# Kernel optimization log

Measured on AMD Instinct MI355X. Metric: run time of the kernel, lower is better.

## Reference

```python
import jax, jax.numpy as jnp
import numpy as np

B, T_ENC, T_DEC = 32, 128, 32
V_SRC, V_TGT = 32000, 32000
E_SRC, E_TGT = 256, 256
H_ENC, H_DEC, A = 512, 512, 8
CTX = 2 * H_ENC  # bidirectional encoder output dim


def setup_inputs():
    key = jax.random.key(0)
    ks = jax.random.split(key, 24)
    s = jnp.float32(0.02)

    def rn(k, shape):
        return jax.random.normal(k, shape, jnp.float32) * s

    return {
        'encoder_inputs': jax.random.randint(ks[0], (B, T_ENC), 0, V_SRC),
        'encoder_seq_length': jax.random.randint(ks[1], (B,), 1, T_ENC + 1),
        'decoder_inputs': jax.random.randint(ks[2], (B, T_DEC), 0, V_TGT),
        'decoder_seq_length': jax.random.randint(ks[3], (B,), 1, T_DEC + 1),
        'emb_src': rn(ks[4], (V_SRC, E_SRC)).at[0].set(0.0),  # padding_idx=0
        'emb_tgt': rn(ks[5], (V_TGT, E_TGT)).at[0].set(0.0),
        'Wih_f': rn(ks[6], (4 * H_ENC, E_SRC)), 'Whh_f': rn(ks[7], (4 * H_ENC, H_ENC)),
        'bih_f': rn(ks[8], (4 * H_ENC,)), 'bhh_f': rn(ks[9], (4 * H_ENC,)),
        'Wih_b': rn(ks[10], (4 * H_ENC, E_SRC)), 'Whh_b': rn(ks[11], (4 * H_ENC, H_ENC)),
        'bih_b': rn(ks[12], (4 * H_ENC,)), 'bhh_b': rn(ks[13], (4 * H_ENC,)),
        'gru_Wih': rn(ks[14], (3 * H_DEC, E_TGT + CTX)), 'gru_Whh': rn(ks[15], (3 * H_DEC, H_DEC)),
        'gru_bih': rn(ks[16], (3 * H_DEC,)), 'gru_bhh': rn(ks[17], (3 * H_DEC,)),
        'attn_W': rn(ks[18], (CTX + H_DEC, A)), 'attn_b': rn(ks[19], (A,)),
        'attn_v': rn(ks[20], (A,)),
        'clf_W': rn(ks[21], (V_TGT, H_DEC)), 'clf_b': rn(ks[22], (V_TGT,)),
    }


def _lstm(x_tbe, Wih, Whh, bih, bhh):
    # x_tbe: [T, B, E] -> hidden outputs [T, B, H]; PyTorch gate order i,f,g,o
    Bz = x_tbe.shape[1]
    h0 = jnp.zeros((Bz, H_ENC), x_tbe.dtype)

    def step(carry, xt):
        h, c = carry
        g = xt @ Wih.T + bih + h @ Whh.T + bhh
        i, f, gg, o = jnp.split(g, 4, axis=-1)
        c = jax.nn.sigmoid(f) * c + jax.nn.sigmoid(i) * jnp.tanh(gg)
        h = jax.nn.sigmoid(o) * jnp.tanh(c)
        return (h, c), h

    _, hs = jax.lax.scan(step, (h0, h0), x_tbe)
    return hs


def _gru(x, h, Wih, Whh, bih, bhh):
    # PyTorch GRUCell: gates r, z, n
    gi = x @ Wih.T + bih
    gh = h @ Whh.T + bhh
    ir, iz, inn = jnp.split(gi, 3, axis=-1)
    hr, hz, hn = jnp.split(gh, 3, axis=-1)
    r = jax.nn.sigmoid(ir + hr)
    z = jax.nn.sigmoid(iz + hz)
    n = jnp.tanh(inn + r * hn)
    return (1.0 - z) * n + z * h


def reference(encoder_inputs, encoder_seq_length, decoder_inputs, decoder_seq_length,
              emb_src, emb_tgt,
              Wih_f, Whh_f, bih_f, bhh_f, Wih_b, Whh_b, bih_b, bhh_b,
              gru_Wih, gru_Whh, gru_bih, gru_bhh,
              attn_W, attn_b, attn_v, clf_W, clf_b):
    lens = encoder_seq_length
    x = emb_src[encoder_inputs]                                   # [B,T,E]
    t = jnp.arange(T_ENC)[None, :]
    valid = t < lens[:, None]                                     # [B,T]

    # forward LSTM (padded steps masked out below; they never affect valid outputs)
    h_f = jnp.swapaxes(_lstm(jnp.swapaxes(x, 0, 1), Wih_f, Whh_f, bih_f, bhh_f), 0, 1)
    # backward LSTM: reverse each sequence within its true length
    rev = jnp.where(valid, lens[:, None] - 1 - t, t)              # [B,T]
    x_r = jnp.take_along_axis(x, rev[:, :, None], axis=1)
    h_b = jnp.swapaxes(_lstm(jnp.swapaxes(x_r, 0, 1), Wih_b, Whh_b, bih_b, bhh_b), 0, 1)
    h_b = jnp.take_along_axis(h_b, rev[:, :, None], axis=1)
    # pad_packed_sequence zeroes outputs past seq length
    enc_out = jnp.concatenate([h_f, h_b], axis=-1) * valid[:, :, None].astype(x.dtype)  # [B,T,2H]

    NEG = jnp.float32(-1e9)

    def step(h, tok):
        # ConcatAttention: v^T tanh(W [enc_out; state] + b), masked softmax
        feat = jnp.concatenate(
            [enc_out, jnp.broadcast_to(h[:, None, :], (B, T_ENC, H_DEC))], axis=-1)
        e = jnp.tanh(feat @ attn_W + attn_b) @ attn_v             # [B,T]
        a = jax.nn.softmax(jnp.where(valid, e, NEG), axis=-1)
        ctx = jnp.einsum('bt,btd->bd', a, enc_out)                # [B,2H]
        # pre-concat decoder: GRUCell([emb; ctx], h)
        xin = jnp.concatenate([emb_tgt[tok], ctx], axis=-1)
        h_new = _gru(xin, h, gru_Wih, gru_Whh, gru_bih, gru_bhh)
        logit = jax.nn.relu(h_new @ clf_W.T + clf_b)              # [B,V]
        return h_new, logit

    h0 = jnp.zeros((B, H_DEC), jnp.float32)
    _, outs = jax.lax.scan(step, h0, jnp.swapaxes(decoder_inputs, 0, 1))
    return jnp.swapaxes(outs, 0, 1)                               # [B,T_dec,V_tgt]
```

## Files before the change

kernel.cpp:

```cpp
#include <hip/hip_runtime.h>
#include <cmath>

#define NB   32
#define TE   128
#define TD   32
#define VOC  32000
#define EMB  256
#define HH   512
#define CTXD 1024
#define NR   1536

#define OHS  8192
#define OEO  (OHS + 2*129*NB*HH)
#define OEP  (OEO + NB*TE*CTXD)
#define OHD  (OEP + NB*TE*8)
#define OVEO (OHD + (TD+1)*NB*HH)
#define WSEND (OVEO + NB*NR*TE/2)

typedef __attribute__((ext_vector_type(8))) short bf16x8;
typedef __attribute__((ext_vector_type(4))) float f32x4;

__device__ __forceinline__ float sigf(float x) { return 1.0f / (1.0f + expf(-x)); }
__device__ __forceinline__ float hsum4(float4 v) { return (v.x + v.y) + (v.z + v.w); }

__device__ __forceinline__ void stg1(float* p, float v) {
  __hip_atomic_store(p, v, __ATOMIC_RELAXED, __HIP_MEMORY_SCOPE_AGENT);
}

__device__ __forceinline__ void fma4(float4& a, const float4 w, const float4 u) {
  a.x = fmaf(w.x, u.x, a.x); a.y = fmaf(w.y, u.y, a.y);
  a.z = fmaf(w.z, u.z, a.z); a.w = fmaf(w.w, u.w, a.w);
}

__device__ __forceinline__ unsigned short to_bf16(float f) {
  unsigned int u = __float_as_uint(f);
  u = (u + 0x7FFF + ((u >> 16) & 1)) >> 16;
  return (unsigned short)u;
}

__device__ __forceinline__ void gbarG(int* bar, int idx, int target) {
  __syncthreads();
  if (threadIdx.x == 0) {
    __hip_atomic_fetch_add(bar + (idx & 7) * 16, 1,
                           __ATOMIC_RELAXED, __HIP_MEMORY_SCOPE_AGENT);
  }
  if (threadIdx.x < 64) {
    const int ln = threadIdx.x;
    int it = 0;
    while (true) {
      int v = (ln < 8)
        ? __hip_atomic_load(bar + ln * 16, __ATOMIC_RELAXED, __HIP_MEMORY_SCOPE_AGENT)
        : 0;
      v += __shfl_xor(v, 1); v += __shfl_xor(v, 2); v += __shfl_xor(v, 4);
      v = __shfl(v, 0);
      if (v >= target) break;
      __builtin_amdgcn_s_sleep(1);
      if (++it > (1 << 20)) break;
    }
  }
  __syncthreads();
}

__global__ void __launch_bounds__(512)
scan_kernel(const int* __restrict__ enc_in, const int* __restrict__ lens,
            const float* __restrict__ emb_src,
            const float* __restrict__ Wih_f, const float* __restrict__ Whh_f,
            const float* __restrict__ bih_f, const float* __restrict__ bhh_f,
            const float* __restrict__ Wih_b, const float* __restrict__ Whh_b,
            const float* __restrict__ bih_b, const float* __restrict__ bhh_b,
            float* __restrict__ ws)
{
  const int tid = threadIdx.x, bid = blockIdx.x;
  const int g = bid & 7, cg = bid >> 3;
  const int dir = g >> 2, bg = g & 3;
  int* flg = (int*)ws + g * 512;
  float* harr = ws + OHS;
  float* eo   = ws + OEO;

  asm volatile("buffer_inv sc1" ::: "memory");

  __shared__ int   tokL[TE][8];
  __shared__ float lds_p[8][4][68];

  for (int i = tid; i < TE * 8; i += 512) {
    int bb = i & 7, s = i >> 3;
    int b = bg * 8 + bb;
    int t = s;
    if (dir) { int L = lens[b]; t = (s < L) ? (L - 1 - s) : s; }
    tokL[s][bb] = enc_in[b * TE + t];
  }
  if (tid < 128) {
    int bb = tid >> 4, col = tid & 15;
    stg1(&harr[((size_t)(dir * 129) * NB + bg * 8 + bb) * HH + cg * 16 + col], 0.0f);
  }

  const int lane = tid & 63, w = tid >> 6;
  const int ks = w & 3, rh = w >> 2;
  const int rq = lane >> 4, kl = lane & 15;
  const int j0 = cg * 16;
  const float* Wih = dir ? Wih_b : Wih_f;
  const float* Whh = dir ? Whh_b : Whh_f;

  float4 Wreg[8][3];
  #pragma unroll
  for (int ri = 0; ri < 8; ++ri) {
    int r = rh * 32 + rq * 8 + ri;
    int o = (r >> 4) * HH + j0 + (r & 15);
    #pragma unroll
    for (int p = 0; p < 3; ++p) {
      int kf = (ks * 3 + p) * 16 + kl;
      Wreg[ri][p] = (kf < 64)
        ? *((const float4*)Wih + (size_t)o * 64 + kf)
        : *((const float4*)Whh + (size_t)o * 128 + (kf - 64));
    }
  }

  const int b_u = tid >> 4, col_u = tid & 15;
  const int j_u = j0 + col_u;
  const int bglob = bg * 8 + b_u;
  const int Lu = (tid < 128) ? lens[bglob] : 0;
  float bs0 = 0, bs1 = 0, bs2 = 0, bs3 = 0;
  if (tid < 128) {
    const float* bih = dir ? bih_b : bih_f;
    const float* bhh = dir ? bhh_b : bhh_f;
    bs0 = bih[j_u] + bhh[j_u];
    bs1 = bih[HH + j_u] + bhh[HH + j_u];
    bs2 = bih[2 * HH + j_u] + bhh[2 * HH + j_u];
    bs3 = bih[3 * HH + j_u] + bhh[3 * HH + j_u];
  }
  float cst = 0.0f;

  const int pbase = (ks == 1) ? 0 : (ks == 2) ? 8 : 20;
  const int pnum  = (ks == 1) ? 8 : 12;

  __syncthreads();
  if (tid == 0)
    __hip_atomic_store(flg + cg * 16, 1, __ATOMIC_RELAXED, __HIP_MEMORY_SCOPE_AGENT);

  for (int s = 0; s < TE; ++s) {
    if (ks != 0) {
      int it = 0;
      while (true) {
        int v = (lane < pnum)
          ? __hip_atomic_load(flg + (pbase + lane) * 16,
                              __ATOMIC_RELAXED, __HIP_MEMORY_SCOPE_AGENT)
          : 0x7fffffff;
        v = min(v, __shfl_xor(v, 1));  v = min(v, __shfl_xor(v, 2));
        v = min(v, __shfl_xor(v, 4));  v = min(v, __shfl_xor(v, 8));
        v = min(v, __shfl_xor(v, 16)); v = min(v, __shfl_xor(v, 32));
        if (v >= s + 1) break;
        __builtin_amdgcn_s_sleep(1);
        if (++it > (1 << 20)) break;
      }
    }

    const float4* h4 = (const float4*)(harr + ((size_t)(dir * 129 + s) * NB) * HH);
    #pragma unroll 2
    for (int bb = 0; bb < 8; ++bb) {
      const int b = bg * 8 + bb;
      const int tok = tokL[s][bb];
      const float4* x4 = (const float4*)emb_src + (size_t)tok * 64;
      float4 u[3];
      #pragma unroll
      for (int p = 0; p < 3; ++p) {
        int c = ks * 3 + p;
        u[p] = (c < 4) ? x4[c * 16 + kl]
                       : h4[(size_t)b * 128 + (c - 4) * 16 + kl];
      }
      float sc[8];
      #pragma unroll
      for (int ri = 0; ri < 8; ++ri) {
        float4 a = {0, 0, 0, 0};
        fma4(a, Wreg[ri][0], u[0]);
        fma4(a, Wreg[ri][1], u[1]);
        fma4(a, Wreg[ri][2], u[2]);
        sc[ri] = hsum4(a);
      }
      #pragma unroll
      for (int ri = 0; ri < 8; ++ri) {
        sc[ri] += __shfl_xor(sc[ri], 1);
        sc[ri] += __shfl_xor(sc[ri], 2);
        sc[ri] += __shfl_xor(sc[ri], 4);
        sc[ri] += __shfl_xor(sc[ri], 8);
      }
      if (kl == 0) {
        int r0 = rh * 32 + rq * 8;
        float4 lo = {sc[0], sc[1], sc[2], sc[3]};
        float4 hi = {sc[4], sc[5], sc[6], sc[7]};
        *(float4*)&lds_p[bb][ks][r0]     = lo;
        *(float4*)&lds_p[bb][ks][r0 + 4] = hi;
      }
    }
    __syncthreads();

    if (tid < 128) {
      float gi = bs0, gf = bs1, gg = bs2, go = bs3;
      #pragma unroll
      for (int k2 = 0; k2 < 4; ++k2) {
        gi += lds_p[b_u][k2][col_u];
        gf += lds_p[b_u][k2][16 + col_u];
        gg += lds_p[b_u][k2][32 + col_u];
        go += lds_p[b_u][k2][48 + col_u];
      }
      float c = sigf(gf) * cst + sigf(gi) * tanhf(gg);
      cst = c;
      float h = sigf(go) * tanhf(c);
      stg1(&harr[((size_t)(dir * 129 + s + 1) * NB + bglob) * HH + j_u], h);
      float hm = (s < Lu) ? h : 0.0f;
      int pos = dir ? ((s < Lu) ? (Lu - 1 - s) : s) : s;
      eo[((size_t)bglob * TE + pos) * CTXD + dir * HH + j_u] = hm;
    }
    __syncthreads();
    if (tid == 0)
      __hip_atomic_store(flg + cg * 16, s + 2,
                         __ATOMIC_RELAXED, __HIP_MEMORY_SCOPE_AGENT);
  }
}

__global__ void __launch_bounds__(256)
veo_kernel(const float* __restrict__ eo, const float* __restrict__ gWih,
           unsigned short* __restrict__ veo)
{
  asm volatile("buffer_inv sc1" ::: "memory");
  __shared__ __align__(16) float As[16][132];
  __shared__ __align__(16) float Bs[16][132];
  const int tid = threadIdx.x;
  const int tx = tid & 15, ty = tid >> 4;
  const int n0 = blockIdx.x * 128, m0 = blockIdx.y * 128;
  float acc[8][8] = {};
  const int lr = tid >> 1;
  const int lk = (tid & 1) * 8;
  const float* arow = eo + (size_t)(m0 + lr) * CTXD;
  const float* brow = gWih + (size_t)(n0 + lr) * (EMB + CTXD) + EMB;

  for (int kc = 0; kc < CTXD; kc += 16) {
    float4 av0 = *(const float4*)&arow[kc + lk];
    float4 av1 = *(const float4*)&arow[kc + lk + 4];
    float4 bv0 = *(const float4*)&brow[kc + lk];
    float4 bv1 = *(const float4*)&brow[kc + lk + 4];
    __syncthreads();
    As[lk + 0][lr] = av0.x; As[lk + 1][lr] = av0.y;
    As[lk + 2][lr] = av0.z; As[lk + 3][lr] = av0.w;
    As[lk + 4][lr] = av1.x; As[lk + 5][lr] = av1.y;
    As[lk + 6][lr] = av1.z; As[lk + 7][lr] = av1.w;
    Bs[lk + 0][lr] = bv0.x; Bs[lk + 1][lr] = bv0.y;
    Bs[lk + 2][lr] = bv0.z; Bs[lk + 3][lr] = bv0.w;
    Bs[lk + 4][lr] = bv1.x; Bs[lk + 5][lr] = bv1.y;
    Bs[lk + 6][lr] = bv1.z; Bs[lk + 7][lr] = bv1.w;
    __syncthreads();
    #pragma unroll
    for (int kk = 0; kk < 16; ++kk) {
      float a8[8], b8[8];
      *(float4*)&a8[0] = *(const float4*)&As[kk][ty * 8];
      *(float4*)&a8[4] = *(const float4*)&As[kk][ty * 8 + 4];
      *(float4*)&b8[0] = *(const float4*)&Bs[kk][tx * 8];
      *(float4*)&b8[4] = *(const float4*)&Bs[kk][tx * 8 + 4];
      #pragma unroll
      for (int i = 0; i < 8; ++i)
        #pragma unroll
        for (int j = 0; j < 8; ++j)
          acc[i][j] = fmaf(a8[i], b8[j], acc[i][j]);
    }
  }
  const int b = m0 >> 7;
  #pragma unroll
  for (int j = 0; j < 8; ++j) {
    int n = n0 + tx * 8 + j;
    unsigned short o8[8];
    #pragma unroll
    for (int i = 0; i < 8; ++i) o8[i] = to_bf16(acc[i][j]);
    *(uint4*)&veo[((size_t)b * NR + n) * TE + ty * 8] = *(uint4*)o8;
  }
}

__global__ void __launch_bounds__(512)
dec_kernel(const int* __restrict__ dec_in, const int* __restrict__ lens,
           const float* __restrict__ emb_tgt,
           const float* __restrict__ gWih, const float* __restrict__ gWhh,
           const float* __restrict__ gbih, const float* __restrict__ gbhh,
           const float* __restrict__ attn_W, const float* __restrict__ attn_b,
           const float* __restrict__ attn_v,
           float* __restrict__ ws)
{
  const int tid = threadIdx.x, bid = blockIdx.x;
  const int g = bid & 7, cg = bid >> 3;
  const int B4 = g * 4;
  int* bar = (int*)ws + 4096 + g * 128;
  float* eo = ws + OEO;
  float* ep = ws + OEP;
  float* hd = ws + OHD;
  const unsigned short* veoH = (const unsigned short*)(ws + OVEO);

  asm volatile("buffer_inv sc1" ::: "memory");

  __shared__ float hl[4][520];
  __shared__ int   tokD[TD][4];
  __shared__ int   lensh[4];
  __shared__ float av8v[8];
  __shared__ float hpv[4][8];
  __shared__ float elds[4][128];
  __shared__ float wlds[4][128];
  __shared__ float mxs[4], invs[4];
  __shared__ float gvc[4][48];
  __shared__ float lds_pd[2][4][4][52];

  for (int i = tid; i < TD * 4; i += 512)
    tokD[i >> 2][i & 3] = dec_in[(B4 + (i & 3)) * TD + (i >> 2)];
  if (tid < 8) av8v[tid] = attn_v[tid];
  if (tid < 4) lensh[tid] = lens[B4 + tid];

  if (tid < 64) {
    int bb = tid >> 4, col = tid & 15;
    stg1(&hd[(size_t)(B4 + bb) * HH + cg * 16 + col], 0.0f);
  }

  {
    const int idx = cg * 512 + tid;
    if (idx < 4 * TE * 8) {
      int a = idx & 7, t = (idx >> 3) & 127, bb = idx >> 10;
      int b = B4 + bb;
      float acc = attn_b[a];
      const float* er = &eo[((size_t)b * TE + t) * CTXD];
      for (int d = 0; d < CTXD; d += 4) {
        float4 ev = *(const float4*)&er[d];
        acc = fmaf(ev.x, attn_W[(d + 0) * 8 + a], acc);
        acc = fmaf(ev.y, attn_W[(d + 1) * 8 + a], acc);
        acc = fmaf(ev.z, attn_W[(d + 2) * 8 + a], acc);
        acc = fmaf(ev.w, attn_W[(d + 3) * 8 + a], acc);
      }
      stg1(&ep[((size_t)b * TE + t) * 8 + a], acc);
    }
  }

  const int lane = tid & 63, w = tid >> 6;
  const int ks = w & 3, rh = w >> 2;
  const int rq = lane >> 4, kl = lane & 15;
  float4 Wreg[6][3];
  #pragma unroll
  for (int ri = 0; ri < 6; ++ri) {
    int rr = rh * 24 + rq * 6 + ri;
    int row = (rr >> 4) * HH + cg * 16 + (rr & 15);
    #pragma unroll
    for (int p = 0; p < 3; ++p) {
      int c = ks * 3 + p;
      Wreg[ri][p] = (c < 4)
        ? *(const float4*)(gWih + (size_t)row * (EMB + CTXD) + c * 64 + kl * 4)
        : *(const float4*)(gWhh + (size_t)row * HH + (c - 4) * 64 + kl * 4);
    }
  }

  const int ub = tid >> 4, ucol = tid & 15;
  const int uj = cg * 16 + ucol;
  float bRc = 0, bZc = 0, bNi = 0, bNh = 0;
  if (tid < 64) {
    bRc = gbih[uj] + gbhh[uj];
    bZc = gbih[HH + uj] + gbhh[HH + uj];
    bNi = gbih[2 * HH + uj];
    bNh = gbhh[2 * HH + uj];
  }

  int tgt = 32;
  gbarG(bar, cg, tgt); tgt += 32;

  for (int s = 0; s < TD; ++s) {
    {
      int bb = tid >> 7, c4 = (tid & 127) * 4;
      *(float4*)&hl[bb][c4] =
        *(const float4*)&hd[((size_t)s * NB + B4 + bb) * HH + c4];
    }
    __syncthreads();
    {
      const int bb = w >> 1;
      const float4* h4 = (const float4*)&hl[bb][0];
      float4 ha = h4[lane * 2], hb = h4[lane * 2 + 1];
      #pragma unroll
      for (int i = 0; i < 4; ++i) {
        const int a = (w & 1) * 4 + i;
        const float* wa = attn_W + (size_t)(CTXD + lane * 8) * 8 + a;
        float acc = 0.0f;
        acc = fmaf(ha.x, wa[0],  acc); acc = fmaf(ha.y, wa[8],  acc);
        acc = fmaf(ha.z, wa[16], acc); acc = fmaf(ha.w, wa[24], acc);
        acc = fmaf(hb.x, wa[32], acc); acc = fmaf(hb.y, wa[40], acc);
        acc = fmaf(hb.z, wa[48], acc); acc = fmaf(hb.w, wa[56], acc);
        acc += __shfl_xor(acc, 1);  acc += __shfl_xor(acc, 2);
        acc += __shfl_xor(acc, 4);  acc += __shfl_xor(acc, 8);
        acc += __shfl_xor(acc, 16); acc += __shfl_xor(acc, 32);
        if (lane == 0) hpv[bb][a] = acc;
      }
    }
    __syncthreads();
    {
      const int bb = tid >> 7, t = tid & 127;
      const int b = B4 + bb;
      float evv = -1e9f;
      if (t < lensh[bb]) {
        const float* e8 = &ep[((size_t)b * TE + t) * 8];
        float4 ea = *(const float4*)e8, eb2 = *(const float4*)(e8 + 4);
        evv  = tanhf(ea.x + hpv[bb][0]) * av8v[0];
        evv += tanhf(ea.y + hpv[bb][1]) * av8v[1];
        evv += tanhf(ea.z + hpv[bb][2]) * av8v[2];
        evv += tanhf(ea.w + hpv[bb][3]) * av8v[3];
        evv += tanhf(eb2.x + hpv[bb][4]) * av8v[4];
        evv += tanhf(eb2.y + hpv[bb][5]) * av8v[5];
        evv += tanhf(eb2.z + hpv[bb][6]) * av8v[6];
        evv += tanhf(eb2.w + hpv[bb][7]) * av8v[7];
      }
      elds[bb][t] = evv;
    }
    __syncthreads();
    if (tid < 256) {
      const int bb = tid >> 6, i = tid & 63;
      float m = fmaxf(elds[bb][i], elds[bb][i + 64]);
      m = fmaxf(m, __shfl_xor(m, 1));  m = fmaxf(m, __shfl_xor(m, 2));
      m = fmaxf(m, __shfl_xor(m, 4));  m = fmaxf(m, __shfl_xor(m, 8));
      m = fmaxf(m, __shfl_xor(m, 16)); m = fmaxf(m, __shfl_xor(m, 32));
      if (i == 0) mxs[bb] = m;
    }
    __syncthreads();
    {
      const int bb = tid >> 7, t = tid & 127;
      wlds[bb][t] = expf(elds[bb][t] - mxs[bb]);
    }
    __syncthreads();
    if (tid < 256) {
      const int bb = tid >> 6, i = tid & 63;
      float sm = wlds[bb][i] + wlds[bb][i + 64];
      sm += __shfl_xor(sm, 1);  sm += __shfl_xor(sm, 2);
      sm += __shfl_xor(sm, 4);  sm += __shfl_xor(sm, 8);
      sm += __shfl_xor(sm, 16); sm += __shfl_xor(sm, 32);
      if (i == 0) invs[bb] = 1.0f / sm;
    }
    {
      #pragma unroll
      for (int bb = 0; bb < 4; ++bb) {
        const float4* xr = (const float4*)(emb_tgt + (size_t)tokD[s][bb] * EMB);
        float4 u[3];
        #pragma unroll
        for (int p = 0; p < 3; ++p) {
          int c = ks * 3 + p;
          u[p] = (c < 4) ? xr[c * 16 + kl]
                         : *(const float4*)&hl[bb][(c - 4) * 64 + kl * 4];
        }
        float sI[6], sH[6];
        #pragma unroll
        for (int ri = 0; ri < 6; ++ri) {
          float4 aI = {0,0,0,0}, aH = {0,0,0,0};
          #pragma unroll
          for (int p = 0; p < 3; ++p) {
            int c = ks * 3 + p;
            if (c < 4) fma4(aI, Wreg[ri][p], u[p]);
            else       fma4(aH, Wreg[ri][p], u[p]);
          }
          sI[ri] = hsum4(aI); sH[ri] = hsum4(aH);
        }
        #pragma unroll
        for (int ri = 0; ri < 6; ++ri) {
          sI[ri] += __shfl_xor(sI[ri], 1); sH[ri] += __shfl_xor(sH[ri], 1);
          sI[ri] += __shfl_xor(sI[ri], 2); sH[ri] += __shfl_xor(sH[ri], 2);
          sI[ri] += __shfl_xor(sI[ri], 4); sH[ri] += __shfl_xor(sH[ri], 4);
          sI[ri] += __shfl_xor(sI[ri], 8); sH[ri] += __shfl_xor(sH[ri], 8);
        }
        if (kl == 0) {
          int r0 = rh * 24 + rq * 6;
          #pragma unroll
          for (int ri = 0; ri < 6; ++ri) {
            lds_pd[0][bb][ks][r0 + ri] = sI[ri];
            lds_pd[1][bb][ks][r0 + ri] = sH[ri];
          }
        }
      }
    }
    __syncthreads();
    if (tid < 384) {
      const int bb = tid / 96, idx = tid % 96;
      const int rr = idx >> 1, th = idx & 1;
      const int n = (rr >> 4) * HH + cg * 16 + (rr & 15);
      const unsigned short* vp = veoH + ((size_t)(B4 + bb) * NR + n) * TE + th * 64;
      const float* wl = &wlds[bb][th * 64];
      float acc = 0.0f;
      #pragma unroll
      for (int q = 0; q < 8; ++q) {
        uint4 pk = *(const uint4*)&vp[q * 8];
        unsigned int uu[4] = {pk.x, pk.y, pk.z, pk.w};
        #pragma unroll
        for (int h2 = 0; h2 < 4; ++h2) {
          acc = fmaf(wl[q * 8 + h2 * 2 + 0],
                     __uint_as_float((uu[h2] & 0xFFFFu) << 16), acc);
          acc = fmaf(wl[q * 8 + h2 * 2 + 1],
                     __uint_as_float((uu[h2] >> 16) << 16), acc);
        }
      }
      acc += __shfl_xor(acc, 1);
      if (th == 0) gvc[bb][rr] = acc * invs[bb];
    }
    __syncthreads();
    if (tid < 64) {
      float giR = gvc[ub][ucol], ghR = 0;
      float giZ = gvc[ub][16 + ucol], ghZ = 0;
      float giN = gvc[ub][32 + ucol], ghN = 0;
      #pragma unroll
      for (int k2 = 0; k2 < 4; ++k2) {
        giR += lds_pd[0][ub][k2][ucol];      ghR += lds_pd[1][ub][k2][ucol];
        giZ += lds_pd[0][ub][k2][16 + ucol]; ghZ += lds_pd[1][ub][k2][16 + ucol];
        giN += lds_pd[0][ub][k2][32 + ucol]; ghN += lds_pd[1][ub][k2][32 + ucol];
      }
      float r = sigf(giR + ghR + bRc);
      float z = sigf(giZ + ghZ + bZc);
      float n = tanhf(giN + bNi + r * (ghN + bNh));
      float hnew = (1.0f - z) * n + z * hl[ub][uj];
      stg1(&hd[((size_t)(s + 1) * NB + B4 + ub) * HH + uj], hnew);
    }
    gbarG(bar, cg, tgt); tgt += 32;
  }
}

__global__ void __launch_bounds__(256)
conv_kernel(const float* __restrict__ hd,
            unsigned short* __restrict__ Abh, unsigned short* __restrict__ Abl)
{
  asm volatile("buffer_inv sc1" ::: "memory");
  const int idx = blockIdx.x * 256 + threadIdx.x;
  const int m = idx >> 6;
  const int k8 = (idx & 63) * 8;
  const float* src = hd + ((size_t)((m & 31) + 1) * NB + (m >> 5)) * HH + k8;
  float4 a0 = *(const float4*)src;
  float4 a1 = *(const float4*)(src + 4);
  float f[8] = {a0.x, a0.y, a0.z, a0.w, a1.x, a1.y, a1.z, a1.w};
  unsigned short hi[8], lo[8];
  #pragma unroll
  for (int i = 0; i < 8; ++i) {
    unsigned short h = to_bf16(f[i]);
    float fh = __uint_as_float(((unsigned int)h) << 16);
    hi[i] = h;
    lo[i] = to_bf16(f[i] - fh);
  }
  *(uint4*)&Abh[(size_t)m * HH + k8] = *(uint4*)hi;
  *(uint4*)&Abl[(size_t)m * HH + k8] = *(uint4*)lo;
}

__global__ void __launch_bounds__(256)
clf_kernel(const unsigned short* __restrict__ Abh, const unsigned short* __restrict__ Abl,
           const float* __restrict__ W, const float* __restrict__ bias,
           float* __restrict__ out)
{
  asm volatile("buffer_inv sc1" ::: "memory");
  __shared__ __align__(16) unsigned short Ah[256][40];
  __shared__ __align__(16) unsigned short Al[256][40];
  __shared__ __align__(16) unsigned short Wh[128][40];
  const int tid = threadIdx.x;
  const int wv = tid >> 6, l = tid & 63;
  const int lr = l & 15, lkq = l >> 4;
  const int n0 = blockIdx.x * 128, m0 = blockIdx.y * 256;
  f32x4 acc[2][16] = {};

  for (int kc = 0; kc < HH; kc += 32) {
    __syncthreads();
    {
      const unsigned short* sh = Abh + (size_t)(m0 + tid) * HH + kc;
      const unsigned short* sl = Abl + (size_t)(m0 + tid) * HH + kc;
      uint4 h0 = *(const uint4*)(sh);      uint4 h1 = *(const uint4*)(sh + 8);
      uint4 h2 = *(const uint4*)(sh + 16); uint4 h3 = *(const uint4*)(sh + 24);
      uint4 l0 = *(const uint4*)(sl);      uint4 l1 = *(const uint4*)(sl + 8);
      uint4 l2 = *(const uint4*)(sl + 16); uint4 l3 = *(const uint4*)(sl + 24);
      *(uint4*)&Ah[tid][0]  = h0; *(uint4*)&Ah[tid][8]  = h1;
      *(uint4*)&Ah[tid][16] = h2; *(uint4*)&Ah[tid][24] = h3;
      *(uint4*)&Al[tid][0]  = l0; *(uint4*)&Al[tid][8]  = l1;
      *(uint4*)&Al[tid][16] = l2; *(uint4*)&Al[tid][24] = l3;
      const int wr = tid >> 1, hf = tid & 1;
      const float* wsrc = W + (size_t)(n0 + wr) * HH + kc + hf * 16;
      unsigned int o[8];
      #pragma unroll
      for (int i = 0; i < 16; i += 4) {
        float4 v = *(const float4*)&wsrc[i];
        o[(i >> 1) + 0] = (unsigned int)to_bf16(v.x) | ((unsigned int)to_bf16(v.y) << 16);
        o[(i >> 1) + 1] = (unsigned int)to_bf16(v.z) | ((unsigned int)to_bf16(v.w) << 16);
      }
      *(uint4*)&Wh[wr][hf * 16]     = *(uint4*)&o[0];
      *(uint4*)&Wh[wr][hf * 16 + 8] = *(uint4*)&o[4];
    }
    __syncthreads();
    bf16x8 bfr[2];
    bfr[0] = *(const bf16x8*)&Wh[wv * 32 + lr][lkq * 8];
    bfr[1] = *(const bf16x8*)&Wh[wv * 32 + 16 + lr][lkq * 8];
    #pragma unroll
    for (int mf = 0; mf < 16; ++mf) {
      bf16x8 ah = *(const bf16x8*)&Ah[mf * 16 + lr][lkq * 8];
      bf16x8 al = *(const bf16x8*)&Al[mf * 16 + lr][lkq * 8];
      #pragma unroll
      for (int nf = 0; nf < 2; ++nf) {
        acc[nf][mf] = __builtin_amdgcn_mfma_f32_16x16x32_bf16(ah, bfr[nf], acc[nf][mf], 0, 0, 0);
        acc[nf][mf] = __builtin_amdgcn_mfma_f32_16x16x32_bf16(al, bfr[nf], acc[nf][mf], 0, 0, 0);
      }
    }
  }
  #pragma unroll
  for (int nf = 0; nf < 2; ++nf) {
    const int n = n0 + wv * 32 + nf * 16 + lr;
    const float bn = bias[n];
    #pragma unroll
    for (int mf = 0; mf < 16; ++mf) {
      #pragma unroll
      for (int r = 0; r < 4; ++r) {
        int m = m0 + mf * 16 + lkq * 4 + r;
        out[(size_t)m * VOC + n] = fmaxf(acc[nf][mf][r] + bn, 0.0f);
      }
    }
  }
}

extern "C" void kernel_launch(void* const* d_in, const int* in_sizes, int n_in,
                              void* d_out, int out_size, void* d_ws, size_t ws_size,
                              hipStream_t stream)
{
  if (ws_size < (size_t)WSEND * 4) return;

  const int* enc_in  = (const int*)d_in[0];
  const int* enc_len = (const int*)d_in[1];
  const int* dec_in  = (const int*)d_in[2];
  const float* emb_src = (const float*)d_in[4];
  const float* emb_tgt = (const float*)d_in[5];
  const float* Wih_f = (const float*)d_in[6];
  const float* Whh_f = (const float*)d_in[7];
  const float* bih_f = (const float*)d_in[8];
  const float* bhh_f = (const float*)d_in[9];
  const float* Wih_b = (const float*)d_in[10];
  const float* Whh_b = (const float*)d_in[11];
  const float* bih_b = (const float*)d_in[12];
  const float* bhh_b = (const float*)d_in[13];
  const float* gWih  = (const float*)d_in[14];
  const float* gWhh  = (const float*)d_in[15];
  const float* gbih  = (const float*)d_in[16];
  const float* gbhh  = (const float*)d_in[17];
  const float* attn_W = (const float*)d_in[18];
  const float* attn_b = (const float*)d_in[19];
  const float* attn_v = (const float*)d_in[20];
  const float* clf_W = (const float*)d_in[21];
  const float* clf_b = (const float*)d_in[22];
  float* ws  = (float*)d_ws;
  float* out = (float*)d_out;

  unsigned short* Abh = (unsigned short*)(ws + OHS);
  unsigned short* Abl = Abh + (size_t)NB * TD * HH;

  hipMemsetAsync(d_ws, 0, 20480, stream);
  scan_kernel<<<256, 512, 0, stream>>>(enc_in, enc_len, emb_src,
      Wih_f, Whh_f, bih_f, bhh_f, Wih_b, Whh_b, bih_b, bhh_b, ws);
  veo_kernel<<<dim3(NR / 128, (NB * TE) / 128), 256, 0, stream>>>(
      ws + OEO, gWih, (unsigned short*)(ws + OVEO));
  dec_kernel<<<256, 512, 0, stream>>>(dec_in, enc_len, emb_tgt,
      gWih, gWhh, gbih, gbhh, attn_W, attn_b, attn_v, ws);
  conv_kernel<<<256, 256, 0, stream>>>(ws + OHD, Abh, Abl);
  dim3 cg(VOC / 128, (NB * TD) / 256);
  clf_kernel<<<cg, 256, 0, stream>>>(Abh, Abl, clf_W, clf_b, out);
}
```

Before: 2.009 ms.

## Warp-specialize decoder step to overlap attention softmax with GRU dot products

The decoder step is split across warp groups. Warps 0-3 each compute one batch row's attention projection, scores, max and softmax entirely in registers with wave shuffles, while warps 4-7 run their share of the GRU input and hidden dot products. The two groups then swap: warps 0-3 run their GRU dots and warps 4-7 compute the bf16 context projection. This removes several block-wide barriers and LDS round trips per step (the hpv, elds and mxs buffers) and overlaps independent work. The cost is that the context reduction now runs on fewer threads with a longer serial loop, and the two phases may be unevenly balanced.

```diff
diff --git a/kernel.cpp b/kernel.cpp
--- a/kernel.cpp
+++ b/kernel.cpp
@@ -297,10 +297,8 @@
   __shared__ int   tokD[TD][4];
   __shared__ int   lensh[4];
   __shared__ float av8v[8];
-  __shared__ float hpv[4][8];
-  __shared__ float elds[4][128];
   __shared__ float wlds[4][128];
-  __shared__ float mxs[4], invs[4];
+  __shared__ float invs[4];
   __shared__ float gvc[4][48];
   __shared__ float lds_pd[2][4][4][52];
 
@@ -359,6 +357,47 @@
     bNh = gbhh[2 * HH + uj];
   }
 
+  auto DOTS = [&](int s) {
+    #pragma unroll
+    for (int bb = 0; bb < 4; ++bb) {
+      const float4* xr = (const float4*)(emb_tgt + (size_t)tokD[s][bb] * EMB);
+      float4 u[3];
+      #pragma unroll
+      for (int p = 0; p < 3; ++p) {
+        int c = ks * 3 + p;
+        u[p] = (c < 4) ? xr[c * 16 + kl]
+                       : *(const float4*)&hl[bb][(c - 4) * 64 + kl * 4];
+      }
+      float sI[6], sH[6];
+      #pragma unroll
+      for (int ri = 0; ri < 6; ++ri) {
+        float4 aI = {0,0,0,0}, aH = {0,0,0,0};
+        #pragma unroll
+        for (int p = 0; p < 3; ++p) {
+          int c = ks * 3 + p;
+          if (c < 4) fma4(aI, Wreg[ri][p], u[p]);
+          else       fma4(aH, Wreg[ri][p], u[p]);
+        }
+        sI[ri] = hsum4(aI); sH[ri] = hsum4(aH);
+      }
+      #pragma unroll
+      for (int ri = 0; ri < 6; ++ri) {
+        sI[ri] += __shfl_xor(sI[ri], 1); sH[ri] += __shfl_xor(sH[ri], 1);
+        sI[ri] += __shfl_xor(sI[ri], 2); sH[ri] += __shfl_xor(sH[ri], 2);
+        sI[ri] += __shfl_xor(sI[ri], 4); sH[ri] += __shfl_xor(sH[ri], 4);
+        sI[ri] += __shfl_xor(sI[ri], 8); sH[ri] += __shfl_xor(sH[ri], 8);
+      }
+      if (kl == 0) {
+        int r0 = rh * 24 + rq * 6;
+        #pragma unroll
+        for (int ri = 0; ri < 6; ++ri) {
+          lds_pd[0][bb][ks][r0 + ri] = sI[ri];
+          lds_pd[1][bb][ks][r0 + ri] = sH[ri];
+        }
+      }
+    }
+  };
+
   int tgt = 32;
   gbarG(bar, cg, tgt); tgt += 32;
 
@@ -369,13 +408,14 @@
         *(const float4*)&hd[((size_t)s * NB + B4 + bb) * HH + c4];
     }
     __syncthreads();
-    {
-      const int bb = w >> 1;
+
+    if (w < 4) {
+      const int bb = w, b = B4 + bb;
       const float4* h4 = (const float4*)&hl[bb][0];
       float4 ha = h4[lane * 2], hb = h4[lane * 2 + 1];
-      #pragma unroll
-      for (int i = 0; i < 4; ++i) {
-        const int a = (w & 1) * 4 + i;
+      float hp[8];
+      #pragma unroll
+      for (int a = 0; a < 8; ++a) {
         const float* wa = attn_W + (size_t)(CTXD + lane * 8) * 8 + a;
         float acc = 0.0f;
         acc = fmaf(ha.x, wa[0],  acc); acc = fmaf(ha.y, wa[8],  acc);
@@ -385,115 +425,77 @@
         acc += __shfl_xor(acc, 1);  acc += __shfl_xor(acc, 2);
         acc += __shfl_xor(acc, 4);  acc += __shfl_xor(acc, 8);
         acc += __shfl_xor(acc, 16); acc += __shfl_xor(acc, 32);
-        if (lane == 0) hpv[bb][a] = acc;
-      }
-    }
-    __syncthreads();
-    {
-      const int bb = tid >> 7, t = tid & 127;
-      const int b = B4 + bb;
-      float evv = -1e9f;
-      if (t < lensh[bb]) {
-        const float* e8 = &ep[((size_t)b * TE + t) * 8];
+        hp[a] = acc;
+      }
+      const int Lb = lensh[bb];
+      float ev0 = -1e9f, ev1 = -1e9f;
+      if (lane < Lb) {
+        const float* e8 = &ep[((size_t)b * TE + lane) * 8];
         float4 ea = *(const float4*)e8, eb2 = *(const float4*)(e8 + 4);
-        evv  = tanhf(ea.x + hpv[bb][0]) * av8v[0];
-        evv += tanhf(ea.y + hpv[bb][1]) * av8v[1];
-        evv += tanhf(ea.z + hpv[bb][2]) * av8v[2];
-        evv += tanhf(ea.w + hpv[bb][3]) * av8v[3];
-        evv += tanhf(eb2.x + hpv[bb][4]) * av8v[4];
-        evv += tanhf(eb2.y + hpv[bb][5]) * av8v[5];
-        evv += tanhf(eb2.z + hpv[bb][6]) * av8v[6];
-        evv += tanhf(eb2.w + hpv[bb][7]) * av8v[7];
-      }
-      elds[bb][t] = evv;
-    }
-    __syncthreads();
-    if (tid < 256) {
-      const int bb = tid >> 6, i = tid & 63;
-      float m = fmaxf(elds[bb][i], elds[bb][i + 64]);
-      m = fmaxf(m, __shfl_xor(m, 1));  m = fmaxf(m, __shfl_xor(m, 2));
-      m = fmaxf(m, __shfl_xor(m, 4));  m = fmaxf(m, __shfl_xor(m, 8));
-      m = fmaxf(m, __shfl_xor(m, 16)); m = fmaxf(m, __shfl_xor(m, 32));
-      if (i == 0) mxs[bb] = m;
-    }
-    __syncthreads();
-    {
-      const int bb = tid >> 7, t = tid & 127;
-      wlds[bb][t] = expf(elds[bb][t] - mxs[bb]);
-    }
-    __syncthreads();
-    if (tid < 256) {
-      const int bb = tid >> 6, i = tid & 63;
-      float sm = wlds[bb][i] + wlds[bb][i + 64];
+        ev0  = tanhf(ea.x + hp[0]) * av8v[0];
+        ev0 += tanhf(ea.y + hp[1]) * av8v[1];
+        ev0 += tanhf(ea.z + hp[2]) * av8v[2];
+        ev0 += tanhf(ea.w + hp[3]) * av8v[3];
+        ev0 += tanhf(eb2.x + hp[4]) * av8v[4];
+        ev0 += tanhf(eb2.y + hp[5]) * av8v[5];
+        ev0 += tanhf(eb2.z + hp[6]) * av8v[6];
+        ev0 += tanhf(eb2.w + hp[7]) * av8v[7];
+      }
+      if (lane + 64 < Lb) {
+        const float* e8 = &ep[((size_t)b * TE + lane + 64) * 8];
+        float4 ea = *(const float4*)e8, eb2 = *(const float4*)(e8 + 4);
+        ev1  = tanhf(ea.x + hp[0]) * av8v[0];
+        ev1 += tanhf(ea.y + hp[1]) * av8v[1];
+        ev1 += tanhf(ea.z + hp[2]) * av8v[2];
+        ev1 += tanhf(ea.w + hp[3]) * av8v[3];
+        ev1 += tanhf(eb2.x + hp[4]) * av8v[4];
+        ev1 += tanhf(eb2.y + hp[5]) * av8v[5];
+        ev1 += tanhf(eb2.z + hp[6]) * av8v[6];
+        ev1 += tanhf(eb2.w + hp[7]) * av8v[7];
+      }
+      float mx = fmaxf(ev0, ev1);
+      mx = fmaxf(mx, __shfl_xor(mx, 1));  mx = fmaxf(mx, __shfl_xor(mx, 2));
+      mx = fmaxf(mx, __shfl_xor(mx, 4));  mx = fmaxf(mx, __shfl_xor(mx, 8));
+      mx = fmaxf(mx, __shfl_xor(mx, 16)); mx = fmaxf(mx, __shfl_xor(mx, 32));
+      float w0 = expf(ev0 - mx), w1 = expf(ev1 - mx);
+      wlds[bb][lane] = w0;
+      wlds[bb][lane + 64] = w1;
+      float sm = w0 + w1;
       sm += __shfl_xor(sm, 1);  sm += __shfl_xor(sm, 2);
       sm += __shfl_xor(sm, 4);  sm += __shfl_xor(sm, 8);
       sm += __shfl_xor(sm, 16); sm += __shfl_xor(sm, 32);
-      if (i == 0) invs[bb] = 1.0f / sm;
-    }
-    {
-      #pragma unroll
-      for (int bb = 0; bb < 4; ++bb) {
-        const float4* xr = (const float4*)(emb_tgt + (size_t)tokD[s][bb] * EMB);
-        float4 u[3];
+      if (lane == 0) invs[bb] = 1.0f / sm;
+    } else {
+      DOTS(s);
+    }
+    __syncthreads();
+
+    if (w < 4) {
+      DOTS(s);
+    } else {
+      const int bb = w - 4;
+      if (lane < 48) {
+        const int rr = lane;
+        const int n = (rr >> 4) * HH + cg * 16 + (rr & 15);
+        const unsigned short* vp = veoH + ((size_t)(B4 + bb) * NR + n) * TE;
+        float acc = 0.0f;
         #pragma unroll
-        for (int p = 0; p < 3; ++p) {
-          int c = ks * 3 + p;
-          u[p] = (c < 4) ? xr[c * 16 + kl]
-                         : *(const float4*)&hl[bb][(c - 4) * 64 + kl * 4];
-        }
-        float sI[6], sH[6];
-        #pragma unroll
-        for (int ri = 0; ri < 6; ++ri) {
-          float4 aI = {0,0,0,0}, aH = {0,0,0,0};
+        for (int q = 0; q < 16; ++q) {
+          uint4 pk = *(const uint4*)&vp[q * 8];
+          unsigned int uu[4] = {pk.x, pk.y, pk.z, pk.w};
           #pragma unroll
-          for (int p = 0; p < 3; ++p) {
-            int c = ks * 3 + p;
-            if (c < 4) fma4(aI, Wreg[ri][p], u[p]);
-            else       fma4(aH, Wreg[ri][p], u[p]);
-          }
-          sI[ri] = hsum4(aI); sH[ri] = hsum4(aH);
-        }
-        #pragma unroll
-        for (int ri = 0; ri < 6; ++ri) {
-          sI[ri] += __shfl_xor(sI[ri], 1); sH[ri] += __shfl_xor(sH[ri], 1);
-          sI[ri] += __shfl_xor(sI[ri], 2); sH[ri] += __shfl_xor(sH[ri], 2);
-          sI[ri] += __shfl_xor(sI[ri], 4); sH[ri] += __shfl_xor(sH[ri], 4);
-          sI[ri] += __shfl_xor(sI[ri], 8); sH[ri] += __shfl_xor(sH[ri], 8);
-        }
-        if (kl == 0) {
-          int r0 = rh * 24 + rq * 6;
-          #pragma unroll
-          for (int ri = 0; ri < 6; ++ri) {
-            lds_pd[0][bb][ks][r0 + ri] = sI[ri];
-            lds_pd[1][bb][ks][r0 + ri] = sH[ri];
+          for (int h2 = 0; h2 < 4; ++h2) {
+            acc = fmaf(wlds[bb][q * 8 + h2 * 2 + 0],
+                       __uint_as_float((uu[h2] & 0xFFFFu) << 16), acc);
+            acc = fmaf(wlds[bb][q * 8 + h2 * 2 + 1],
+                       __uint_as_float((uu[h2] >> 16) << 16), acc);
           }
         }
-      }
-    }
-    __syncthreads();
-    if (tid < 384) {
-      const int bb = tid / 96, idx = tid % 96;
-      const int rr = idx >> 1, th = idx & 1;
-      const int n = (rr >> 4) * HH + cg * 16 + (rr & 15);
-      const unsigned short* vp = veoH + ((size_t)(B4 + bb) * NR + n) * TE + th * 64;
-      const float* wl = &wlds[bb][th * 64];
-      float acc = 0.0f;
-      #pragma unroll
-      for (int q = 0; q < 8; ++q) {
-        uint4 pk = *(const uint4*)&vp[q * 8];
-        unsigned int uu[4] = {pk.x, pk.y, pk.z, pk.w};
-        #pragma unroll
-        for (int h2 = 0; h2 < 4; ++h2) {
-          acc = fmaf(wl[q * 8 + h2 * 2 + 0],
-                     __uint_as_float((uu[h2] & 0xFFFFu) << 16), acc);
-          acc = fmaf(wl[q * 8 + h2 * 2 + 1],
-                     __uint_as_float((uu[h2] >> 16) << 16), acc);
-        }
-      }
-      acc += __shfl_xor(acc, 1);
-      if (th == 0) gvc[bb][rr] = acc * invs[bb];
-    }
-    __syncthreads();
+        gvc[bb][rr] = acc * invs[bb];
+      }
+    }
+    __syncthreads();
+
     if (tid < 64) {
       float giR = gvc[ub][ucol], ghR = 0;
       float giZ = gvc[ub][16 + ucol], ghZ = 0;
```

Measured after the change: 2.124 ms. +5.7%, slower.
